# Kernel optimization log

Measured on AMD Instinct MI355X. Metric: run time of the kernel, lower is better.

Reference implementation:

```python
import jax, jax.numpy as jnp
import numpy as np

N_NODES = 100000
N_TARGETS = 8192
HIDDEN = 128
HEADS = 4


def setup_inputs() -> dict:
    key = jax.random.key(0)
    ks = iter(jax.random.split(key, 40))
    d = {}
    d['feat0'] = jax.random.normal(next(ks), (50000, 512), jnp.float32)
    d['feat1'] = jax.random.normal(next(ks), (50000, 512), jnp.float32)
    d['node_idx0'] = jnp.arange(50000, dtype=jnp.int32)
    d['node_idx1'] = jnp.arange(50000, dtype=jnp.int32) + 50000
    for nt in ('m', 'd'):
        for p in ('0', '1'):
            d[f'eidx_{nt}{p}'] = jax.random.randint(next(ks), (100000, 3), 0, N_NODES, jnp.int32)
            d[f'etgt_{nt}{p}'] = jax.random.randint(next(ks), (100000,), 0, N_TARGETS, jnp.int32)
    s = lambda *sh: 0.05 * jax.random.normal(next(ks), sh, jnp.float32)
    d['W0'] = s(HIDDEN, 512); d['b0'] = jnp.zeros((HIDDEN,), jnp.float32)
    d['W1'] = s(HIDDEN, 512); d['b1'] = jnp.zeros((HIDDEN,), jnp.float32)
    for nt in ('m', 'd'):
        for p in ('0', '1'):
            d[f'Wr_{nt}{p}'] = s(HEADS * HIDDEN, HIDDEN)
            d[f'a_{nt}{p}'] = s(HEADS, HIDDEN)
        d[f'Ws_{nt}'] = s(128, HEADS * HIDDEN)
        d[f'bs_{nt}'] = jnp.zeros((128,), jnp.float32)
        d[f'vs_{nt}'] = s(128)
        d[f'Wo_{nt}'] = s(64, HEADS * HIDDEN)
        d[f'bo_{nt}'] = jnp.zeros((64,), jnp.float32)
    return d


def _metapath_agg(feats, eidx, etgt, Wr, attn):
    # feats: [N,H]; eidx: [E,L]; etgt: [E] in [0,T)
    E = eidx.shape[0]
    h = feats[eidx].mean(axis=1)                       # [E,H]  metapath-instance encoding ('linear' rnn_type)
    eft = (h @ Wr.T).reshape(E, HEADS, HIDDEN)         # [E,heads,H]
    e = jax.nn.leaky_relu(jnp.einsum('ehd,hd->eh', eft, attn), 0.2)
    m = jax.ops.segment_max(e, etgt, num_segments=N_TARGETS)
    ex = jnp.exp(e - m[etgt])
    den = jax.ops.segment_sum(ex, etgt, num_segments=N_TARGETS)
    alpha = ex / (den[etgt] + 1e-9)                    # segment softmax over instances per target
    out = jax.ops.segment_sum(eft * alpha[:, :, None], etgt, num_segments=N_TARGETS)
    return jax.nn.elu(out).reshape(N_TARGETS, HEADS * HIDDEN)


def _semantic(h_list, Ws, bs, vs):
    betas = jnp.stack([(jnp.tanh(h @ Ws.T + bs) @ vs).mean() for h in h_list])
    beta = jax.nn.softmax(betas)
    return jnp.einsum('p,pth->th', beta, jnp.stack(h_list))


def reference(feat0, feat1, node_idx0, node_idx1,
              eidx_m0, etgt_m0, eidx_m1, etgt_m1,
              eidx_d0, etgt_d0, eidx_d1, etgt_d1,
              W0, b0, W1, b1,
              Wr_m0, a_m0, Wr_m1, a_m1, Wr_d0, a_d0, Wr_d1, a_d1,
              Ws_m, bs_m, vs_m, Ws_d, bs_d, vs_d,
              Wo_m, bo_m, Wo_d, bo_d):
    # per-node-type linear transform scattered by type_mask
    tf = jnp.zeros((N_NODES, HIDDEN), feat0.dtype)
    tf = tf.at[node_idx0].set(feat0 @ W0.T + b0)
    tf = tf.at[node_idx1].set(feat1 @ W1.T + b1)
    # (feat_drop is identity in eval / dropout_rate handled deterministically)
    hm0 = _metapath_agg(tf, eidx_m0, etgt_m0, Wr_m0, a_m0)
    hm1 = _metapath_agg(tf, eidx_m1, etgt_m1, Wr_m1, a_m1)
    hd0 = _metapath_agg(tf, eidx_d0, etgt_d0, Wr_d0, a_d0)
    hd1 = _metapath_agg(tf, eidx_d1, etgt_d1, Wr_d1, a_d1)
    h_miRNA = _semantic([hm0, hm1], Ws_m, bs_m, vs_m)
    h_disease = _semantic([hd0, hd1], Ws_d, bs_d, vs_d)
    logits_miRNA = h_miRNA @ Wo_m.T + bo_m
    logits_disease = h_disease @ Wo_d.T + bo_d
    return (logits_miRNA, logits_disease, h_miRNA, h_disease)
```

## Files before the change

kernel.cpp:

```cpp
#include <hip/hip_runtime.h>
#include <hip/hip_bf16.h>
#include <math.h>


#define HIDDEN 128
#define HEADS 4
#define NTGT 8192
#define NEDGE 100000
#define NNODES 100000

typedef __attribute__((ext_vector_type(8))) short bf16x8;
typedef __attribute__((ext_vector_type(4))) float f32x4;

__device__ inline short b16(float f)
{
    union { __hip_bfloat16 h; short s; } u;
    u.h = __float2bfloat16(f);
    return u.s;
}

__device__ inline float bf2f(unsigned short u)
{
    union { unsigned int i; float f; } v;
    v.i = (unsigned int)u << 16;
    return v.f;
}

__device__ inline void gld_lds16(const void* gsrc, void* ldst)
{
    __builtin_amdgcn_global_load_lds(
        (const __attribute__((address_space(1))) unsigned int*)gsrc,
        (__attribute__((address_space(3))) unsigned int*)ldst, 16, 0, 0);
}

struct GArgs {
    const void* A[4];
    const unsigned short* B[4];
    const float* bias[4];
    void* C[4];
    const int* rowmap[4];
    const float* vs[4];
    float* sem[4];
};

__global__ __launch_bounds__(256)
void tgemm(GArgs g, int M)
{
    __shared__ float lds[32 * 512];
    const int z = blockIdx.z;
    const float* Af = (const float*)g.A[z];
    const unsigned short* Bp = g.B[z];
    const float* bias = g.bias[z];
    const int* rowmap = g.rowmap[z];
    unsigned short* Ch = (unsigned short*)g.C[z];

    const int tid = threadIdx.x;
    const int w = tid >> 6, l = tid & 63;
    const int lr = l & 15, s4 = l >> 4;
    const int m0 = blockIdx.x * 32;

    #pragma unroll
    for (int r8 = 0; r8 < 8; ++r8) {
        int rl = w * 8 + r8;
        int rg = min(m0 + rl, M - 1);
        const float* rowp = Af + (size_t)rg * 512;
        int so = ((l & ~7) | ((l & 7) ^ r8)) * 4;
        gld_lds16(rowp + so, &lds[rl * 512]);
        gld_lds16(rowp + 256 + so, &lds[rl * 512 + 256]);
    }

    const int i = w & 1;
    const int jb = (w >> 1) * 4;

    f32x4 acc[4];
    #pragma unroll
    for (int jj = 0; jj < 4; ++jj) acc[jj] = (f32x4){0.f, 0.f, 0.f, 0.f};

    bf16x8 bbA[4], bbB[4];
    auto LDB = [&](int c, bf16x8 (&bb)[4]) {
        #pragma unroll
        for (int jj = 0; jj < 4; ++jj)
            bb[jj] = *(const bf16x8*)(Bp + ((size_t)(c * 8 + jb + jj) * 64 + l) * 8);
    };

    LDB(0, bbA);
    __syncthreads();

    const int r = i * 16 + lr;
    const int rx = r & 7;

    #pragma unroll
    for (int c = 0; c < 16; ++c) {
        int p0 = c * 8 + ((2 * s4) ^ rx);
        int p1 = c * 8 + ((2 * s4 + 1) ^ rx);
        float4 u = *(const float4*)&lds[r * 512 + p0 * 4];
        float4 v = *(const float4*)&lds[r * 512 + p1 * 4];
        bf16x8 a;
        a[0] = b16(u.x); a[1] = b16(u.y); a[2] = b16(u.z); a[3] = b16(u.w);
        a[4] = b16(v.x); a[5] = b16(v.y); a[6] = b16(v.z); a[7] = b16(v.w);
        if (c & 1) {
            if (c + 1 < 16) LDB(c + 1, bbA);
            #pragma unroll
            for (int jj = 0; jj < 4; ++jj)
                acc[jj] = __builtin_amdgcn_mfma_f32_16x16x32_bf16(a, bbB[jj], acc[jj], 0, 0, 0);
        } else {
            if (c + 1 < 16) LDB(c + 1, bbB);
            #pragma unroll
            for (int jj = 0; jj < 4; ++jj)
                acc[jj] = __builtin_amdgcn_mfma_f32_16x16x32_bf16(a, bbA[jj], acc[jj], 0, 0, 0);
        }
    }

    #pragma unroll
    for (int rr = 0; rr < 4; ++rr) {
        int gm = m0 + i * 16 + s4 * 4 + rr;
        if (gm >= M) continue;
        size_t crow = (size_t)rowmap[gm];
        #pragma unroll
        for (int jj = 0; jj < 4; ++jj) {
            int n = (jb + jj) * 16 + lr;
            Ch[crow * 128 + n] = (unsigned short)b16(acc[jj][rr] + bias[n]);
        }
    }
}

template<int EPI, int NF, int MI, bool AB16, bool C16, int NFS>
__global__ __launch_bounds__(256)
void mgemm(GArgs g, int lda, int ldc,
           int aOffY, int bOffY, int cOffY, int nOffY, int M, int K)
{
    __shared__ float red[4];
    const int z = blockIdx.z;
    const unsigned short* Bp = g.B[z] + (size_t)blockIdx.y * bOffY;
    const float* bias = g.bias[z];
    const int* rowmap = g.rowmap[z];
    const int nbase = blockIdx.y * nOffY;
    float* Cf = nullptr;
    unsigned short* Ch = nullptr;
    if (g.C[z]) {
        if (C16) Ch = (unsigned short*)g.C[z] + (size_t)blockIdx.y * cOffY;
        else     Cf = (float*)g.C[z] + (size_t)blockIdx.y * cOffY;
    }
    const float* Af = nullptr;
    const unsigned short* Ah = nullptr;
    if (AB16) Ah = (const unsigned short*)g.A[z] + (size_t)blockIdx.y * aOffY;
    else      Af = (const float*)g.A[z] + (size_t)blockIdx.y * aOffY;

    const int tid = threadIdx.x;
    const int w = tid >> 6, l = tid & 63;
    const int lr = l & 15, lk = (l >> 4) * 8;
    const int m0 = blockIdx.x * (MI * 64) + w * (MI * 16);

    f32x4 acc[MI][NF];
    #pragma unroll
    for (int i = 0; i < MI; ++i)
        #pragma unroll
        for (int j = 0; j < NF; ++j)
            acc[i][j] = (f32x4){0.f, 0.f, 0.f, 0.f};

    float4 af0[MI][2], af1[MI][2];
    bf16x8 ah0[MI], ah1[MI];
    bf16x8 bb0[NF], bb1[NF];

    auto LD = [&](int k0, float4 (&af)[MI][2], bf16x8 (&ah)[MI], bf16x8 (&bb)[NF]) {
        #pragma unroll
        for (int i = 0; i < MI; ++i) {
            int row = min(m0 + i * 16 + lr, M - 1);
            if (AB16) {
                ah[i] = *(const bf16x8*)(Ah + (size_t)row * lda + k0 + lk);
            } else {
                const float* p = Af + (size_t)row * lda + k0 + lk;
                af[i][0] = *(const float4*)p;
                af[i][1] = *(const float4*)(p + 4);
            }
        }
        #pragma unroll
        for (int j = 0; j < NF; ++j)
            bb[j] = *(const bf16x8*)(Bp + ((size_t)((k0 >> 5) * NFS + j) * 64 + l) * 8);
    };

    auto CMP = [&](float4 (&af)[MI][2], bf16x8 (&ah)[MI], bf16x8 (&bb)[NF]) {
        bf16x8 a[MI];
        #pragma unroll
        for (int i = 0; i < MI; ++i) {
            if (AB16) {
                a[i] = ah[i];
            } else {
                bf16x8 r;
                r[0] = b16(af[i][0].x); r[1] = b16(af[i][0].y);
                r[2] = b16(af[i][0].z); r[3] = b16(af[i][0].w);
                r[4] = b16(af[i][1].x); r[5] = b16(af[i][1].y);
                r[6] = b16(af[i][1].z); r[7] = b16(af[i][1].w);
                a[i] = r;
            }
        }
        #pragma unroll
        for (int j = 0; j < NF; ++j)
            #pragma unroll
            for (int i = 0; i < MI; ++i)
                acc[i][j] = __builtin_amdgcn_mfma_f32_16x16x32_bf16(a[i], bb[j], acc[i][j], 0, 0, 0);
    };

    LD(0, af0, ah0, bb0);
    for (int k0 = 0; k0 < K; k0 += 64) {
        LD(k0 + 32, af1, ah1, bb1);
        CMP(af0, ah0, bb0);
        if (k0 + 64 < K) LD(k0 + 64, af0, ah0, bb0);
        CMP(af1, ah1, bb1);
    }

    if (EPI == 2) {
        const float* vs = g.vs[z];
        float local = 0.f;
        #pragma unroll
        for (int i = 0; i < MI; ++i) {
            int rbase = m0 + i * 16 + (l >> 4) * 4;
            #pragma unroll
            for (int r = 0; r < 4; ++r) {
                if (rbase + r >= M) continue;
                #pragma unroll
                for (int j = 0; j < NF; ++j) {
                    int n = nbase + j * 16 + lr;
                    local += tanhf(acc[i][j][r] + bias[n]) * vs[n];
                }
            }
        }
        #pragma unroll
        for (int o = 32; o; o >>= 1) local += __shfl_xor(local, o, 64);
        if (l == 0) red[w] = local;
        __syncthreads();
        if (tid == 0) atomicAdd(g.sem[z], red[0] + red[1] + red[2] + red[3]);
        return;
    }

    #pragma unroll
    for (int i = 0; i < MI; ++i) {
        int rbase = m0 + i * 16 + (l >> 4) * 4;
        #pragma unroll
        for (int r = 0; r < 4; ++r) {
            int gm = rbase + r;
            if (gm >= M) continue;
            size_t crow = rowmap ? (size_t)rowmap[gm] : (size_t)gm;
            #pragma unroll
            for (int j = 0; j < NF; ++j) {
                int n = nbase + j * 16 + lr;
                float v = acc[i][j][r];
                if (EPI == 0 && bias) v += bias[n];
                if (EPI == 1) v = v > 0.f ? v : expm1f(v);
                if (C16) Ch[crow * (size_t)ldc + n] = (unsigned short)b16(v);
                else     Cf[crow * (size_t)ldc + n] = v;
            }
        }
    }
}

struct PackArgs {
    const float* src[22];
    unsigned short* dst[22];
    int n16[22], k32[22], ld[22];
};

__global__ __launch_bounds__(256)
void pack_kernel(PackArgs pa)
{
    int c = blockIdx.y;
    int idx = blockIdx.x * 256 + threadIdx.x;
    int tot = pa.n16[c] * pa.k32[c] * 64;
    if (idx >= tot) return;
    int l = idx & 63;
    int rest = idx >> 6;
    int j = rest % pa.n16[c];
    int k0 = rest / pa.n16[c];
    int row = j * 16 + (l & 15);
    int col = k0 * 32 + (l >> 4) * 8;
    const float* s = pa.src[c] + (size_t)row * pa.ld[c] + col;
    float4 u = *(const float4*)s;
    float4 v = *(const float4*)(s + 4);
    bf16x8 r;
    r[0] = b16(u.x); r[1] = b16(u.y); r[2] = b16(u.z); r[3] = b16(u.w);
    r[4] = b16(v.x); r[5] = b16(v.y); r[6] = b16(v.z); r[7] = b16(v.w);
    *(bf16x8*)(pa.dst[c] + (size_t)idx * 8) = r;
}

struct WattArgs { const float* Wr[4]; const float* a[4]; };

__global__ __launch_bounds__(256)
void watt_kernel(WattArgs wa, float* __restrict__ watt4)
{
    int idx = blockIdx.x * 256 + threadIdx.x;
    int mp = idx >> 9, rest = idx & 511, h = rest >> 7, k = rest & 127;
    const float* Wr = wa.Wr[mp];
    const float* a = wa.a[mp];
    float s = 0.f;
    #pragma unroll 4
    for (int d = 0; d < HIDDEN; ++d)
        s += a[h * HIDDEN + d] * Wr[(size_t)(h * HIDDEN + d) * HIDDEN + k];
    watt4[idx] = s;
}

__global__ __launch_bounds__(256)
void watt_pack(const float* __restrict__ watt4, unsigned short* __restrict__ dst)
{
    int idx = blockIdx.x * 256 + threadIdx.x;
    int f = idx >> 9;
    int r = idx & 511;
    int l = r >> 3;
    int c = r & 7;
    int row = l & 15;
    int col = f * 32 + ((l >> 4) << 3) + c;
    dst[idx] = (unsigned short)b16(watt4[row * 128 + col]);
}

struct EArgs { const int* eidx[4]; const int* etgt[4]; };

__global__ __launch_bounds__(256)
void hist_kernel(EArgs ea, int* __restrict__ cnt4, int E)
{
    int e = blockIdx.x * 256 + threadIdx.x;
    int mp = blockIdx.y;
    if (e < E) atomicAdd(&cnt4[mp * NTGT + ea.etgt[mp][e]], 1);
}

__global__ __launch_bounds__(256)
void scan_kernel(int* __restrict__ cnt4, int* __restrict__ rowptr4)
{
    int mp = blockIdx.x;
    int* cnt = cnt4 + mp * NTGT;
    int* rowptr = rowptr4 + mp * (NTGT + 1);
    __shared__ int part[256];
    int t = threadIdx.x;
    int vals[32];
    int s = 0;
    int base = t * 32;
    #pragma unroll
    for (int i = 0; i < 32; ++i) { vals[i] = cnt[base + i]; s += vals[i]; }
    part[t] = s;
    __syncthreads();
    for (int o = 1; o < 256; o <<= 1) {
        int v = (t >= o) ? part[t - o] : 0;
        __syncthreads();
        part[t] += v;
        __syncthreads();
    }
    int off = (t == 0) ? 0 : part[t - 1];
    #pragma unroll
    for (int i = 0; i < 32; ++i) { rowptr[base + i] = off; off += vals[i]; cnt[base + i] = 0; }
    if (t == 255) rowptr[NTGT] = off;
}

__global__ __launch_bounds__(256)
void scatter_esc(EArgs ea, const int* __restrict__ rowptr4,
                 int* __restrict__ cur4, uint4* __restrict__ rec4,
                 const float* __restrict__ snode, int E)
{
    int e = blockIdx.x * 256 + threadIdx.x;
    int mp = blockIdx.y;
    if (e >= E) return;
    int t = ea.etgt[mp][e];
    int pos = atomicAdd(&cur4[mp * NTGT + t], 1);
    int slot = rowptr4[mp * (NTGT + 1) + t] + pos;

    const int* eidx = ea.eidx[mp];
    int i0 = eidx[e * 3 + 0], i1 = eidx[e * 3 + 1], i2 = eidx[e * 3 + 2];
    float4 s0 = *(const float4*)(snode + (size_t)i0 * 16 + mp * 4);
    float4 s1 = *(const float4*)(snode + (size_t)i1 * 16 + mp * 4);
    float4 s2 = *(const float4*)(snode + (size_t)i2 * 16 + mp * 4);
    const float inv3 = 1.f / 3.f;
    float es[4];
    es[0] = (s0.x + s1.x + s2.x) * inv3;
    es[1] = (s0.y + s1.y + s2.y) * inv3;
    es[2] = (s0.z + s1.z + s2.z) * inv3;
    es[3] = (s0.w + s1.w + s2.w) * inv3;
    #pragma unroll
    for (int h = 0; h < 4; ++h) {
        float v = (es[h] >= 0.f) ? es[h] : 0.2f * es[h];
        es[h] = __expf(v);
    }
    uint4* rp = rec4 + ((size_t)mp * NEDGE + slot) * 2;
    rp[0] = make_uint4((unsigned)i0, (unsigned)i1, (unsigned)i2, 0u);
    *(float4*)&rp[1] = make_float4(es[0], es[1], es[2], es[3]);
}

__global__ __launch_bounds__(256)
void seg_kernel(const int* __restrict__ rowptr4, const uint4* __restrict__ rec4,
                const unsigned short* __restrict__ tfb,
                unsigned short* __restrict__ gnb)
{
    int mp = blockIdx.y;
    int w = threadIdx.x >> 6, l = threadIdx.x & 63;
    int t = blockIdx.x * 4 + w;
    const int* rp = rowptr4 + mp * (NTGT + 1);
    const uint4* rec = rec4 + (size_t)mp * NEDGE * 2;
    const unsigned short* tfl = tfb + 2 * l;

    int beg = rp[t], end = rp[t + 1];
    int n = end - beg;
    float den[4] = {0, 0, 0, 0}, aa[4] = {0, 0, 0, 0}, ab[4] = {0, 0, 0, 0};
    const float inv3 = 1.f / 3.f;

    if (n > 0) {
        int last = n - 1;
        auto LDI = [&](int j, uint4& ia, float4& wv) {
            int jj = min(j, last);
            ia = rec[(size_t)(beg + jj) * 2];
            wv = *(const float4*)&rec[(size_t)(beg + jj) * 2 + 1];
        };
        uint4 I0, I1, I2, I3, I4;
        float4 W0v, W1v, W2v, W3v, W4v;
        LDI(0, I0, W0v); LDI(1, I1, W1v); LDI(2, I2, W2v); LDI(3, I3, W3v);
        unsigned int x0 = *(const unsigned int*)(tfl + (size_t)I0.x * 128);
        unsigned int x1 = *(const unsigned int*)(tfl + (size_t)I0.y * 128);
        unsigned int x2 = *(const unsigned int*)(tfl + (size_t)I0.z * 128);
        unsigned int y0 = *(const unsigned int*)(tfl + (size_t)I1.x * 128);
        unsigned int y1 = *(const unsigned int*)(tfl + (size_t)I1.y * 128);
        unsigned int y2 = *(const unsigned int*)(tfl + (size_t)I1.z * 128);
        unsigned int z0 = *(const unsigned int*)(tfl + (size_t)I2.x * 128);
        unsigned int z1 = *(const unsigned int*)(tfl + (size_t)I2.y * 128);
        unsigned int z2 = *(const unsigned int*)(tfl + (size_t)I2.z * 128);
        for (int i = 0; i < n; ++i) {
            unsigned int w0 = *(const unsigned int*)(tfl + (size_t)I3.x * 128);
            unsigned int w1 = *(const unsigned int*)(tfl + (size_t)I3.y * 128);
            unsigned int w2 = *(const unsigned int*)(tfl + (size_t)I3.z * 128);
            LDI(i + 4, I4, W4v);
            float fa = (bf2f((unsigned short)x0) + bf2f((unsigned short)x1) +
                        bf2f((unsigned short)x2)) * inv3;
            float fb = (bf2f((unsigned short)(x0 >> 16)) + bf2f((unsigned short)(x1 >> 16)) +
                        bf2f((unsigned short)(x2 >> 16))) * inv3;
            float es[4] = {W0v.x, W0v.y, W0v.z, W0v.w};
            #pragma unroll
            for (int h = 0; h < 4; ++h) {
                den[h] += es[h]; aa[h] += es[h] * fa; ab[h] += es[h] * fb;
            }
            x0 = y0; x1 = y1; x2 = y2;
            y0 = z0; y1 = z1; y2 = z2;
            z0 = w0; z1 = w1; z2 = w2;
            I3 = I4;
            W0v = W1v; W1v = W2v; W2v = W3v; W3v = W4v;
        }
    }

    unsigned short* gr = gnb + ((size_t)mp * NTGT + t) * 512;
    #pragma unroll
    for (int h = 0; h < 4; ++h) {
        float d = 1.f / (den[h] + 1e-9f);
        unsigned int lo = (unsigned int)(unsigned short)b16(aa[h] * d);
        unsigned int hi = (unsigned int)(unsigned short)b16(ab[h] * d);
        *(unsigned int*)(gr + h * 128 + 2 * l) = lo | (hi << 16);
    }
}

__global__ void beta_kernel(const float* __restrict__ s, float* __restrict__ beta)
{
    int nt = threadIdx.x;
    if (nt < 2 && blockIdx.x == 0) {
        float b0 = s[nt * 2] * (1.f / 8192.f), b1 = s[nt * 2 + 1] * (1.f / 8192.f);
        float mm = fmaxf(b0, b1);
        float e0 = __expf(b0 - mm), e1 = __expf(b1 - mm);
        float d = e0 + e1;
        beta[nt * 2] = e0 / d;
        beta[nt * 2 + 1] = e1 / d;
    }
}

__global__ __launch_bounds__(256)
void combine_kernel(const unsigned short* __restrict__ obb,
                    const float* __restrict__ betab,
                    float* __restrict__ hout, unsigned short* __restrict__ hb)
{
    int nt = blockIdx.y;
    size_t i4 = ((size_t)blockIdx.x * 256 + threadIdx.x) * 4;
    const unsigned short* o0 = obb + (size_t)(2 * nt) * NTGT * 512 + i4;
    const unsigned short* o1 = obb + (size_t)(2 * nt + 1) * NTGT * 512 + i4;
    float b0 = betab[nt * 2], b1 = betab[nt * 2 + 1];
    uint2 xa = *(const uint2*)o0;
    uint2 xb = *(const uint2*)o1;
    float4 r;
    r.x = b0 * bf2f((unsigned short)xa.x)         + b1 * bf2f((unsigned short)xb.x);
    r.y = b0 * bf2f((unsigned short)(xa.x >> 16)) + b1 * bf2f((unsigned short)(xb.x >> 16));
    r.z = b0 * bf2f((unsigned short)xa.y)         + b1 * bf2f((unsigned short)xb.y);
    r.w = b0 * bf2f((unsigned short)(xa.y >> 16)) + b1 * bf2f((unsigned short)(xb.y >> 16));
    *(float4*)(hout + (size_t)nt * NTGT * 512 + i4) = r;
    unsigned int lo = (unsigned int)(unsigned short)b16(r.x) |
                      ((unsigned int)(unsigned short)b16(r.y) << 16);
    unsigned int hi = (unsigned int)(unsigned short)b16(r.z) |
                      ((unsigned int)(unsigned short)b16(r.w) << 16);
    *(uint2*)(hb + (size_t)nt * NTGT * 512 + i4) = make_uint2(lo, hi);
}

extern "C" void kernel_launch(void* const* d_in, const int* in_sizes, int n_in,
                              void* d_out, int out_size, void* d_ws, size_t ws_size,
                              hipStream_t stream)
{
    const float* feat0 = (const float*)d_in[0];
    const float* feat1 = (const float*)d_in[1];
    const int* nidx0 = (const int*)d_in[2];
    const int* nidx1 = (const int*)d_in[3];
    const int* eidx[4] = {(const int*)d_in[4], (const int*)d_in[6],
                          (const int*)d_in[8], (const int*)d_in[10]};
    const int* etgt[4] = {(const int*)d_in[5], (const int*)d_in[7],
                          (const int*)d_in[9], (const int*)d_in[11]};
    const float* W0 = (const float*)d_in[12]; const float* b0 = (const float*)d_in[13];
    const float* W1 = (const float*)d_in[14]; const float* b1 = (const float*)d_in[15];
    const float* Wr[4] = {(const float*)d_in[16], (const float*)d_in[18],
                          (const float*)d_in[25], (const float*)d_in[27]};
    const float* av[4] = {(const float*)d_in[17], (const float*)d_in[19],
                          (const float*)d_in[26], (const float*)d_in[28]};
    const float* Ws[2] = {(const float*)d_in[20], (const float*)d_in[29]};
    const float* bs[2] = {(const float*)d_in[21], (const float*)d_in[30]};
    const float* vsem[2] = {(const float*)d_in[22], (const float*)d_in[31]};
    const float* Wo[2] = {(const float*)d_in[23], (const float*)d_in[32]};
    const float* bo[2] = {(const float*)d_in[24], (const float*)d_in[33]};
    float* out = (float*)d_out;

    char* p = (char*)d_ws;
    auto carve = [&](size_t bytes) { char* r = p; p += (bytes + 255) & ~(size_t)255; return r; };
    unsigned short* tfb = (unsigned short*)carve((size_t)NNODES * 128 * 2);
    unsigned short* gnb = (unsigned short*)carve((size_t)4 * NTGT * 512 * 2);
    unsigned short* obb = (unsigned short*)carve((size_t)4 * NTGT * 512 * 2);
    unsigned short* hb  = (unsigned short*)carve((size_t)2 * NTGT * 512 * 2);
    float* snode        = (float*)carve((size_t)NNODES * 16 * 4);
    uint4* rec4         = (uint4*)carve((size_t)4 * NEDGE * 32);
    unsigned short* w0b = (unsigned short*)carve(65536 * 2);
    unsigned short* w1b = (unsigned short*)carve(65536 * 2);
    unsigned short* wrb = (unsigned short*)carve(4 * 65536 * 2);
    unsigned short* wsb = (unsigned short*)carve(2 * 65536 * 2);
    unsigned short* wob = (unsigned short*)carve(2 * 32768 * 2);
    unsigned short* wattp = (unsigned short*)carve(2048 * 2);
    float* watt4        = (float*)carve(4 * 512 * 4);
    float* ssem         = (float*)carve(4 * 4);
    float* betab        = (float*)carve(4 * 4);
    int* cnt4           = (int*)carve((size_t)4 * NTGT * 4);
    int* rowptr4        = (int*)carve((size_t)4 * (NTGT + 1) * 4);

    hipMemsetAsync(ssem, 0, 16, stream);
    hipMemsetAsync(cnt4, 0, (size_t)4 * NTGT * 4, stream);

    dim3 blk(256, 1, 1);

    PackArgs pa;
    pa.src[0] = W0; pa.dst[0] = w0b; pa.n16[0] = 8; pa.k32[0] = 16; pa.ld[0] = 512;
    pa.src[1] = W1; pa.dst[1] = w1b; pa.n16[1] = 8; pa.k32[1] = 16; pa.ld[1] = 512;
    for (int mp = 0; mp < 4; ++mp)
        for (int h = 0; h < 4; ++h) {
            int c = 2 + mp * 4 + h;
            pa.src[c] = Wr[mp] + (size_t)h * 128 * 128;
            pa.dst[c] = wrb + (size_t)(mp * 4 + h) * 16384;
            pa.n16[c] = 8; pa.k32[c] = 4; pa.ld[c] = 128;
        }
    pa.src[18] = Ws[0]; pa.dst[18] = wsb;         pa.n16[18] = 8; pa.k32[18] = 16; pa.ld[18] = 512;
    pa.src[19] = Ws[1]; pa.dst[19] = wsb + 65536; pa.n16[19] = 8; pa.k32[19] = 16; pa.ld[19] = 512;
    pa.src[20] = Wo[0]; pa.dst[20] = wob;         pa.n16[20] = 4; pa.k32[20] = 16; pa.ld[20] = 512;
    pa.src[21] = Wo[1]; pa.dst[21] = wob + 32768; pa.n16[21] = 4; pa.k32[21] = 16; pa.ld[21] = 512;
    pack_kernel<<<dim3(32, 22), blk, 0, stream>>>(pa);

    WattArgs wa;
    for (int mp = 0; mp < 4; ++mp) { wa.Wr[mp] = Wr[mp]; wa.a[mp] = av[mp]; }
    watt_kernel<<<dim3(8), blk, 0, stream>>>(wa, watt4);
    watt_pack<<<dim3(8), blk, 0, stream>>>(watt4, wattp);

    {
        GArgs g = {};
        g.A[0] = feat0; g.A[1] = feat1;
        g.B[0] = w0b;   g.B[1] = w1b;
        g.bias[0] = b0; g.bias[1] = b1;
        g.C[0] = tfb;   g.C[1] = tfb;
        g.rowmap[0] = nidx0; g.rowmap[1] = nidx1;
        tgemm<<<dim3(1563, 1, 2), blk, 0, stream>>>(g, 50000);
    }

    {
        GArgs g = {};
        g.A[0] = tfb;
        g.B[0] = wattp;
        g.C[0] = snode;
        mgemm<0, 1, 2, true, false, 1><<<dim3(782, 1, 1), blk, 0, stream>>>(
            g, 128, 16, 0, 0, 0, 0, NNODES, 128);
    }

    EArgs ea;
    for (int mp = 0; mp < 4; ++mp) { ea.eidx[mp] = eidx[mp]; ea.etgt[mp] = etgt[mp]; }

    hist_kernel<<<dim3(391, 4), blk, 0, stream>>>(ea, cnt4, NEDGE);
    scan_kernel<<<dim3(4), blk, 0, stream>>>(cnt4, rowptr4);
    scatter_esc<<<dim3(391, 4), blk, 0, stream>>>(ea, rowptr4, cnt4, rec4,
                                                  snode, NEDGE);
    seg_kernel<<<dim3(NTGT / 4, 4), blk, 0, stream>>>(rowptr4, rec4, tfb, gnb);

    const size_t LOG_OFF[2] = {0, (size_t)NTGT * 64};
    float* hout = out + (size_t)NTGT * 128;

    {
        GArgs g = {};
        for (int mp = 0; mp < 4; ++mp) {
            g.A[mp] = gnb + (size_t)mp * NTGT * 512;
            g.B[mp] = wrb + (size_t)mp * 65536;
            g.C[mp] = obb + (size_t)mp * NTGT * 512;
        }
        mgemm<1, 8, 2, true, true, 8><<<dim3(64, 4, 4), blk, 0, stream>>>(
            g, 512, 512, 128, 16384, 128, 0, NTGT, 128);
    }

    {
        GArgs g = {};
        for (int mp = 0; mp < 4; ++mp) {
            int nt = mp >> 1;
            g.A[mp] = obb + (size_t)mp * NTGT * 512;
            g.B[mp] = wsb + (size_t)nt * 65536;
            g.bias[mp] = bs[nt];
            g.vs[mp] = vsem[nt];
            g.sem[mp] = ssem + mp;
        }
        mgemm<2, 4, 1, true, false, 8><<<dim3(128, 2, 4), blk, 0, stream>>>(
            g, 512, 0, 0, 2048, 0, 64, NTGT, 512);
    }

    beta_kernel<<<dim3(1), dim3(64), 0, stream>>>(ssem, betab);
    combine_kernel<<<dim3(NTGT * 512 / 4 / 256, 2), blk, 0, stream>>>(obb, betab, hout, hb);

    {
        GArgs g = {};
        for (int nt = 0; nt < 2; ++nt) {
            g.A[nt] = hb + (size_t)nt * NTGT * 512;
            g.B[nt] = wob + (size_t)nt * 32768;
            g.bias[nt] = bo[nt];
            g.C[nt] = out + LOG_OFF[nt];
        }
        mgemm<0, 2, 1, true, false, 4><<<dim3(128, 2, 2), blk, 0, stream>>>(
            g, 512, 64, 0, 1024, 0, 32, NTGT, 512);
    }
}
```

Before: 293.5 us.

## Convert A tile to bf16 during staging to halve LDS footprint

Replaces the direct global-to-LDS fp32 loads with register loads that convert to bf16 before writing into a swizzled bf16 LDS tile. LDS use per block drops from 64KB to 32KB, and launch bounds now ask for 4 blocks per SM to raise occupancy. Each A element is converted once rather than once per reading wave, and the MFMA operand now comes from a single 16-byte LDS read. The cost is that the asynchronous global_load_lds path is lost, so loads now pass through registers and register pressure rises.

```diff
diff --git a/kernel.cpp b/kernel.cpp
--- a/kernel.cpp
+++ b/kernel.cpp
@@ -24,13 +24,6 @@
     union { unsigned int i; float f; } v;
     v.i = (unsigned int)u << 16;
     return v.f;
-}
-
-__device__ inline void gld_lds16(const void* gsrc, void* ldst)
-{
-    __builtin_amdgcn_global_load_lds(
-        (const __attribute__((address_space(1))) unsigned int*)gsrc,
-        (__attribute__((address_space(3))) unsigned int*)ldst, 16, 0, 0);
 }
 
 struct GArgs {
@@ -43,10 +36,10 @@
     float* sem[4];
 };
 
-__global__ __launch_bounds__(256)
+__global__ __launch_bounds__(256, 4)
 void tgemm(GArgs g, int M)
 {
-    __shared__ float lds[32 * 512];
+    __shared__ unsigned short lds[32 * 512];
     const int z = blockIdx.z;
     const float* Af = (const float*)g.A[z];
     const unsigned short* Bp = g.B[z];
@@ -59,15 +52,34 @@
     const int lr = l & 15, s4 = l >> 4;
     const int m0 = blockIdx.x * 32;
 
-    #pragma unroll
-    for (int r8 = 0; r8 < 8; ++r8) {
-        int rl = w * 8 + r8;
-        int rg = min(m0 + rl, M - 1);
-        const float* rowp = Af + (size_t)rg * 512;
-        int so = ((l & ~7) | ((l & 7) ^ r8)) * 4;
-        gld_lds16(rowp + so, &lds[rl * 512]);
-        gld_lds16(rowp + 256 + so, &lds[rl * 512 + 256]);
-    }
+    auto stage4 = [&](int rbase) {
+        float4 v[4][2];
+        #pragma unroll
+        for (int q = 0; q < 4; ++q) {
+            int rg = min(m0 + rbase + q, M - 1);
+            const float* rowp = Af + (size_t)rg * 512;
+            v[q][0] = *(const float4*)(rowp + l * 4);
+            v[q][1] = *(const float4*)(rowp + 256 + l * 4);
+        }
+        #pragma unroll
+        for (int q = 0; q < 4; ++q) {
+            int rl = rbase + q;
+            int rx = rl & 7;
+            #pragma unroll
+            for (int hh = 0; hh < 2; ++hh) {
+                uint2 pk;
+                pk.x = (unsigned int)(unsigned short)b16(v[q][hh].x) |
+                       ((unsigned int)(unsigned short)b16(v[q][hh].y) << 16);
+                pk.y = (unsigned int)(unsigned short)b16(v[q][hh].z) |
+                       ((unsigned int)(unsigned short)b16(v[q][hh].w) << 16);
+                int G = hh * 32 + (l >> 1);
+                int slot = (G & ~7) | ((G & 7) ^ rx);
+                *(uint2*)((char*)lds + (size_t)rl * 1024 + slot * 16 + (l & 1) * 8) = pk;
+            }
+        }
+    };
+    stage4(w * 8);
+    stage4(w * 8 + 4);
 
     const int i = w & 1;
     const int jb = (w >> 1) * 4;
@@ -91,13 +103,9 @@
 
     #pragma unroll
     for (int c = 0; c < 16; ++c) {
-        int p0 = c * 8 + ((2 * s4) ^ rx);
-        int p1 = c * 8 + ((2 * s4 + 1) ^ rx);
-        float4 u = *(const float4*)&lds[r * 512 + p0 * 4];
-        float4 v = *(const float4*)&lds[r * 512 + p1 * 4];
-        bf16x8 a;
-        a[0] = b16(u.x); a[1] = b16(u.y); a[2] = b16(u.z); a[3] = b16(u.w);
-        a[4] = b16(v.x); a[5] = b16(v.y); a[6] = b16(v.z); a[7] = b16(v.w);
+        int G = 4 * c + s4;
+        int slot = (G & ~7) | ((G & 7) ^ rx);
+        bf16x8 a = *(const bf16x8*)((const char*)lds + (size_t)r * 1024 + slot * 16);
         if (c & 1) {
             if (c + 1 < 16) LDB(c + 1, bbA);
             #pragma unroll
```

Result: no change. 292.7 us (-0.3%).
